# Kernel optimization log

Measured on AMD Instinct MI355X. Metric: run time of the kernel, lower is better.

## Reference

```python
import jax, jax.numpy as jnp
import numpy as np

B, S, D, F, E, K = 4, 2048, 512, 2048, 8, 2


def setup_inputs() -> dict:
    key = jax.random.key(0)
    kx, kg, kw, kv, k2 = jax.random.split(key, 5)
    scale = 0.02
    return {
        "x": jax.random.normal(kx, (B, S, D), dtype=jnp.float32),
        "Wg": jax.random.normal(kg, (D, E), dtype=jnp.float32) * scale,
        "W": jax.random.normal(kw, (E, D, F), dtype=jnp.float32) * scale,
        "V": jax.random.normal(kv, (E, D, F), dtype=jnp.float32) * scale,
        "W2": jax.random.normal(k2, (E, F, D), dtype=jnp.float32) * scale,
    }


def reference(x, Wg, W, V, W2):
    # Gating: top-k over expert logits, softmax over the selected k logits.
    gate_logits = jnp.einsum("bsd,de->bse", x, Wg)                 # [B,S,E]
    topv, topi = jax.lax.top_k(gate_logits, K)                      # [B,S,K]
    w = jax.nn.softmax(topv, axis=-1)                               # [B,S,K]
    # Dense per-token combine weights: gw[b,s,e] = sum_k w[b,s,k]*[topi[b,s,k]==e]
    gw = jnp.sum(w[..., None] * jax.nn.one_hot(topi, E, dtype=x.dtype), axis=-2)  # [B,S,E]

    y = jnp.zeros_like(x)
    n_experts = W.shape[0]
    for e in range(n_experts):  # fixed small loop over experts
        h = jax.nn.silu(jnp.einsum("bsd,df->bsf", x, W[e])) * jnp.einsum("bsd,df->bsf", x, V[e])
        y = y + gw[..., e:e + 1] * jnp.einsum("bsf,fd->bsd", h, W2[e])
    return y
```

## Files before the change

kernel.cpp:

```cpp
#include <hip/hip_runtime.h>
#include <hip/hip_bf16.h>
#include <stdint.h>

#define TT 8192
#define DD 512
#define FF 2048
#define EE 8
#define MAXT 136

typedef __attribute__((ext_vector_type(8))) short bf16x8;
typedef __attribute__((ext_vector_type(4))) float f32x4;

static __device__ __forceinline__ unsigned short f2b(float f) {
  union { __hip_bfloat16 b; unsigned short u; } cv;
  cv.b = __float2bfloat16(f);
  return cv.u;
}

static __device__ __forceinline__ void gload16(const void* g, void* l) {
  __builtin_amdgcn_global_load_lds(
      (const __attribute__((address_space(1))) unsigned int*)g,
      (__attribute__((address_space(3))) unsigned int*)l, 16, 0, 0);
}

__launch_bounds__(256)
__global__ void k_prep(const float* __restrict__ x, const float* __restrict__ Wg,
                       unsigned short* __restrict__ xb,
                       int* __restrict__ te, float* __restrict__ tw) {
  int wid = threadIdx.x >> 6, lane = threadIdx.x & 63;
  int t = blockIdx.x * 4 + wid;
  const float* xr = x + (size_t)t * DD;
  unsigned short* xbr = xb + (size_t)t * DD;
  int d0 = lane * 8;

  float4 v0 = *(const float4*)(xr + d0);
  float4 v1 = *(const float4*)(xr + d0 + 4);
  ushort4 o0, o1;
  o0.x = f2b(v0.x); o0.y = f2b(v0.y); o0.z = f2b(v0.z); o0.w = f2b(v0.w);
  o1.x = f2b(v1.x); o1.y = f2b(v1.y); o1.z = f2b(v1.z); o1.w = f2b(v1.w);
  *(ushort4*)(xbr + d0) = o0;
  *(ushort4*)(xbr + d0 + 4) = o1;

  float xv[8] = {v0.x, v0.y, v0.z, v0.w, v1.x, v1.y, v1.z, v1.w};
  float acc[EE];
#pragma unroll
  for (int e = 0; e < EE; e++) acc[e] = 0.f;
#pragma unroll
  for (int j = 0; j < 8; j++) {
    const float* wg = Wg + (size_t)(d0 + j) * EE;
    float4 a = *(const float4*)wg;
    float4 b = *(const float4*)(wg + 4);
    acc[0] += xv[j] * a.x; acc[1] += xv[j] * a.y; acc[2] += xv[j] * a.z; acc[3] += xv[j] * a.w;
    acc[4] += xv[j] * b.x; acc[5] += xv[j] * b.y; acc[6] += xv[j] * b.z; acc[7] += xv[j] * b.w;
  }
#pragma unroll
  for (int e = 0; e < EE; e++)
    for (int o = 32; o; o >>= 1) acc[e] += __shfl_xor(acc[e], o);
  if (lane == 0) {
    int e1 = 0; float v1m = acc[0];
#pragma unroll
    for (int e = 1; e < EE; e++) if (acc[e] > v1m) { v1m = acc[e]; e1 = e; }
    int e2 = -1; float v2m = -INFINITY;
#pragma unroll
    for (int e = 0; e < EE; e++) if (e != e1 && acc[e] > v2m) { v2m = acc[e]; e2 = e; }
    float ex = __expf(v2m - v1m);
    float w1 = 1.f / (1.f + ex);
    float w2 = ex / (1.f + ex);
    te[t * 2] = e1; te[t * 2 + 1] = e2;
    tw[t * 2] = w1; tw[t * 2 + 1] = w2;
  }
}

__global__ void k_tcvt_all(const float* __restrict__ W, const float* __restrict__ V,
                           const float* __restrict__ W2, unsigned short* __restrict__ Wt,
                           unsigned short* __restrict__ Vt, unsigned short* __restrict__ W2t) {
  __shared__ float tile[32][33];
  int z = blockIdx.y;
  const float* src; unsigned short* dst; int N, nbx;
  if (z < 16) {
    int e = z & 7;
    size_t base = (size_t)e * DD * FF;
    src = (z < 8 ? W : V) + base;
    dst = (z < 8 ? Wt : Vt) + base;
    N = FF; nbx = FF / 32;
  } else {
    int e = z - 16;
    size_t base = (size_t)e * DD * FF;
    src = W2 + base; dst = W2t + base;
    N = DD; nbx = DD / 32;
  }
  int M = (z < 16) ? DD : FF;
  int bx = blockIdx.x;
  int cb = (bx % nbx) * 32, rb = (bx / nbx) * 32;
  int tx = threadIdx.x, ty = threadIdx.y;
#pragma unroll
  for (int i = 0; i < 4; i++)
    tile[ty + i * 8][tx] = src[(size_t)(rb + ty + i * 8) * N + cb + tx];
  __syncthreads();
#pragma unroll
  for (int i = 0; i < 4; i++)
    dst[(size_t)(cb + ty + i * 8) * M + rb + tx] = f2b(tile[tx][ty + i * 8]);
}

__launch_bounds__(1024)
__global__ void k_route(const int* __restrict__ te, const float* __restrict__ tw,
                        int* __restrict__ ctrl, int* __restrict__ perm,
                        float* __restrict__ pw, int* __restrict__ tileE,
                        int* __restrict__ tileRow, int* __restrict__ inv) {
  __shared__ int wsum[17][EE];
  __shared__ int ebase[EE];
  int tid = threadIdx.x;
  int lane = tid & 63, wid = tid >> 6;
  int myte[16]; float mytw[16];
  int c[EE];
#pragma unroll
  for (int e = 0; e < EE; e++) c[e] = 0;
  int s0 = tid * 16;
#pragma unroll
  for (int j = 0; j < 16; j++) {
    myte[j] = te[s0 + j];
    mytw[j] = tw[s0 + j];
#pragma unroll
    for (int e = 0; e < EE; e++) if (myte[j] == e) c[e]++;
  }
  int incl[EE];
#pragma unroll
  for (int e = 0; e < EE; e++) incl[e] = c[e];
  for (int off = 1; off < 64; off <<= 1) {
#pragma unroll
    for (int e = 0; e < EE; e++) {
      int v = __shfl_up(incl[e], off);
      if (lane >= off) incl[e] += v;
    }
  }
  if (lane == 63)
#pragma unroll
    for (int e = 0; e < EE; e++) wsum[wid][e] = incl[e];
  __syncthreads();
  if (tid < EE) {
    int s = 0;
    for (int w = 0; w < 16; w++) { int v = wsum[w][tid]; wsum[w][tid] = s; s += v; }
    wsum[16][tid] = s;
  }
  __syncthreads();
  if (tid == 0) {
    int s = 0, nt = 0;
    for (int e = 0; e < EE; e++) {
      int cnt = wsum[16][e];
      ebase[e] = s; ctrl[8 + e] = s; ctrl[e] = cnt;
      for (int i = 0; i < cnt; i += 128) { tileE[nt] = e; tileRow[nt] = s + i; nt++; }
      s += cnt;
    }
    ctrl[16] = s; ctrl[17] = nt;
  }
  __syncthreads();
#pragma unroll
  for (int e = 0; e < EE; e++) {
    int p = ebase[e] + wsum[wid][e] + incl[e] - c[e];
#pragma unroll
    for (int j = 0; j < 16; j++) {
      if (myte[j] == e) {
        perm[p] = (s0 + j) >> 1;
        pw[p] = mytw[j];
        inv[s0 + j] = p;
        p++;
      }
    }
  }
}

__launch_bounds__(256, 2)
__global__ void k_ffn1(const unsigned short* __restrict__ xb,
                       const unsigned short* __restrict__ Wt,
                       const unsigned short* __restrict__ Vt,
                       const int* __restrict__ perm, const float* __restrict__ pw,
                       const int* __restrict__ ctrl, const int* __restrict__ tileE,
                       const int* __restrict__ tileRow,
                       unsigned short* __restrict__ h) {
  int ti = blockIdx.y;
  if (ti >= ctrl[17]) return;
  int e = tileE[ti];
  int row0 = tileRow[ti];
  int last = ctrl[8 + e] + ctrl[e] - 1;
  int f0 = blockIdx.x * 128;

  __shared__ __align__(16) short As[2][128 * 32];
  __shared__ __align__(16) short Bs[2][256 * 32];

  int tid = threadIdx.x;
  int lane = tid & 63, wid = tid >> 6;
  int wr = wid >> 1, wc = wid & 1;

  int sl = (((tid & 3) ^ ((tid >> 3) & 3))) * 8;

  int ar1 = row0 + (tid >> 2); if (ar1 > last) ar1 = last;
  int ar2 = row0 + (tid >> 2) + 64; if (ar2 > last) ar2 = last;
  const unsigned short* agp1 = xb + (size_t)perm[ar1] * DD + sl;
  const unsigned short* agp2 = xb + (size_t)perm[ar2] * DD + sl;
  const unsigned short* wgp1 = Wt + ((size_t)e * FF + f0 + (tid >> 2)) * DD + sl;
  const unsigned short* wgp2 = wgp1 + (size_t)64 * DD;
  const unsigned short* vgp1 = Vt + ((size_t)e * FF + f0 + (tid >> 2)) * DD + sl;
  const unsigned short* vgp2 = vgp1 + (size_t)64 * DD;

#define STAGE1(buf, k0) do { \
    gload16(agp1 + (k0), &As[buf][tid * 8]); \
    gload16(agp2 + (k0), &As[buf][(tid + 256) * 8]); \
    gload16(wgp1 + (k0), &Bs[buf][tid * 8]); \
    gload16(wgp2 + (k0), &Bs[buf][(tid + 256) * 8]); \
    gload16(vgp1 + (k0), &Bs[buf][(tid + 512) * 8]); \
    gload16(vgp2 + (k0), &Bs[buf][(tid + 768) * 8]); \
  } while (0)

  f32x4 zz = {0.f, 0.f, 0.f, 0.f};
  f32x4 accw[4][4], accv[4][4];
#pragma unroll
  for (int m = 0; m < 4; m++)
#pragma unroll
    for (int n = 0; n < 4; n++) { accw[m][n] = zz; accv[m][n] = zz; }

  int lrow = lane & 15;
  int jx = (((lane >> 4) ^ ((lane >> 1) & 3))) * 8;

#define COMP1(buf) do { \
    bf16x8 a[4], bw[4], bv[4]; \
    _Pragma("unroll") \
    for (int m = 0; m < 4; m++) a[m] = *(bf16x8*)&As[buf][(wr * 64 + m * 16 + lrow) * 32 + jx]; \
    _Pragma("unroll") \
    for (int n = 0; n < 4; n++) { \
      bw[n] = *(bf16x8*)&Bs[buf][(wc * 64 + n * 16 + lrow) * 32 + jx]; \
      bv[n] = *(bf16x8*)&Bs[buf][(128 + wc * 64 + n * 16 + lrow) * 32 + jx]; \
    } \
    _Pragma("unroll") \
    for (int m = 0; m < 4; m++) \
      _Pragma("unroll") \
      for (int n = 0; n < 4; n++) { \
        accw[m][n] = __builtin_amdgcn_mfma_f32_16x16x32_bf16(a[m], bw[n], accw[m][n], 0, 0, 0); \
        accv[m][n] = __builtin_amdgcn_mfma_f32_16x16x32_bf16(a[m], bv[n], accv[m][n], 0, 0, 0); \
      } \
  } while (0)

  STAGE1(0, 0);
  __syncthreads();
#pragma unroll 1
  for (int ks = 0; ks < 16; ks += 2) {
    if (ks + 1 < 16) STAGE1(1, (ks + 1) * 32);
    COMP1(0);
    __syncthreads();
    if (ks + 2 < 16) STAGE1(0, (ks + 2) * 32);
    COMP1(1);
    __syncthreads();
  }
#undef STAGE1
#undef COMP1

#pragma unroll
  for (int m = 0; m < 4; m++) {
    int rbase = row0 + wr * 64 + m * 16 + (lane >> 4) * 4;
#pragma unroll
    for (int reg = 0; reg < 4; reg++) {
      int r = rbase + reg;
      if (r > last) continue;
      float pwv = pw[r];
      size_t hrow = (size_t)r * FF;
#pragma unroll
      for (int n = 0; n < 4; n++) {
        float a = accw[m][n][reg];
        float b = accv[m][n][reg];
        float hv = a / (1.f + __expf(-a)) * b * pwv;
        h[hrow + f0 + wc * 64 + n * 16 + lrow] = f2b(hv);
      }
    }
  }
}

__launch_bounds__(256)
__global__ void k_ffn2(const unsigned short* __restrict__ h,
                       const unsigned short* __restrict__ W2t,
                       const int* __restrict__ ctrl,
                       const int* __restrict__ tileE, const int* __restrict__ tileRow,
                       float* __restrict__ yp) {
  int ti = blockIdx.y;
  if (ti >= ctrl[17]) return;
  int e = tileE[ti];
  int row0 = tileRow[ti];
  int last = ctrl[8 + e] + ctrl[e] - 1;
  int d0 = blockIdx.x * 128;

  __shared__ __align__(16) short As[2][128 * 32];
  __shared__ __align__(16) short Bs[2][128 * 32];

  int tid = threadIdx.x;
  int lane = tid & 63, wid = tid >> 6;
  int wm = (wid >> 1) * 64, wn = (wid & 1) * 64;

  int sl = (((tid & 3) ^ ((tid >> 3) & 3))) * 8;

  int ar1 = row0 + (tid >> 2); if (ar1 > last) ar1 = last;
  int ar2 = row0 + (tid >> 2) + 64; if (ar2 > last) ar2 = last;
  const unsigned short* agp1 = h + (size_t)ar1 * FF + sl;
  const unsigned short* agp2 = h + (size_t)ar2 * FF + sl;
  const unsigned short* bgp1 = W2t + ((size_t)e * DD + d0 + (tid >> 2)) * FF + sl;
  const unsigned short* bgp2 = bgp1 + (size_t)64 * FF;

#define STAGE2(buf, k0) do { \
    gload16(agp1 + (k0), &As[buf][tid * 8]); \
    gload16(agp2 + (k0), &As[buf][(tid + 256) * 8]); \
    gload16(bgp1 + (k0), &Bs[buf][tid * 8]); \
    gload16(bgp2 + (k0), &Bs[buf][(tid + 256) * 8]); \
  } while (0)

  f32x4 zz = {0.f, 0.f, 0.f, 0.f};
  f32x4 acc[4][4];
#pragma unroll
  for (int m = 0; m < 4; m++)
#pragma unroll
    for (int n = 0; n < 4; n++) acc[m][n] = zz;

  int lrow = lane & 15;
  int jx = (((lane >> 4) ^ ((lane >> 1) & 3))) * 8;

#define COMP2(buf) do { \
    bf16x8 a[4], b[4]; \
    _Pragma("unroll") \
    for (int m = 0; m < 4; m++) a[m] = *(bf16x8*)&As[buf][(wm + m * 16 + lrow) * 32 + jx]; \
    _Pragma("unroll") \
    for (int n = 0; n < 4; n++) b[n] = *(bf16x8*)&Bs[buf][(wn + n * 16 + lrow) * 32 + jx]; \
    _Pragma("unroll") \
    for (int m = 0; m < 4; m++) \
      _Pragma("unroll") \
      for (int n = 0; n < 4; n++) \
        acc[m][n] = __builtin_amdgcn_mfma_f32_16x16x32_bf16(a[m], b[n], acc[m][n], 0, 0, 0); \
  } while (0)

  STAGE2(0, 0);
  __syncthreads();
#pragma unroll 1
  for (int ks = 0; ks < 64; ks += 2) {
    if (ks + 1 < 64) STAGE2(1, (ks + 1) * 32);
    COMP2(0);
    __syncthreads();
    if (ks + 2 < 64) STAGE2(0, (ks + 2) * 32);
    COMP2(1);
    __syncthreads();
  }
#undef STAGE2
#undef COMP2

#pragma unroll
  for (int m = 0; m < 4; m++) {
    int rbase = row0 + wm + m * 16 + (lane >> 4) * 4;
#pragma unroll
    for (int reg = 0; reg < 4; reg++) {
      int r = rbase + reg;
      if (r > last) continue;
      float* ypr = yp + (size_t)r * DD + d0;
#pragma unroll
      for (int n = 0; n < 4; n++)
        ypr[wn + n * 16 + lrow] = acc[m][n][reg];
    }
  }
}

__launch_bounds__(256)
__global__ void k_gather(const float4* __restrict__ yp4, const int* __restrict__ inv,
                         float4* __restrict__ y4) {
  int i = blockIdx.x * 256 + threadIdx.x;
  int t = i >> 7, c = i & 127;
  int pa = inv[2 * t], pb = inv[2 * t + 1];
  float4 a = yp4[(size_t)pa * 128 + c];
  float4 b = yp4[(size_t)pb * 128 + c];
  float4 o;
  o.x = a.x + b.x; o.y = a.y + b.y; o.z = a.z + b.z; o.w = a.w + b.w;
  y4[i] = o;
}

extern "C" void kernel_launch(void* const* d_in, const int* in_sizes, int n_in,
                              void* d_out, int out_size, void* d_ws, size_t ws_size,
                              hipStream_t stream) {
  const float* x  = (const float*)d_in[0];
  const float* Wg = (const float*)d_in[1];
  const float* W  = (const float*)d_in[2];
  const float* V  = (const float*)d_in[3];
  const float* W2 = (const float*)d_in[4];
  float* y = (float*)d_out;

  char* ws = (char*)d_ws;
  size_t off = 0;
  auto alloc = [&](size_t n) -> char* {
    char* p = ws + off;
    off += (n + 255) & ~(size_t)255;
    return p;
  };
  unsigned short* xb  = (unsigned short*)alloc((size_t)TT * DD * 2);
  unsigned short* Wt  = (unsigned short*)alloc((size_t)EE * DD * FF * 2);
  unsigned short* Vt  = (unsigned short*)alloc((size_t)EE * DD * FF * 2);
  unsigned short* W2t = (unsigned short*)alloc((size_t)EE * DD * FF * 2);
  unsigned short* h   = (unsigned short*)alloc((size_t)TT * 2 * FF * 2);
  int*   perm = (int*)alloc(TT * 2 * 4);
  float* pw   = (float*)alloc(TT * 2 * 4);
  int*   te   = (int*)alloc(TT * 2 * 4);
  float* tw   = (float*)alloc(TT * 2 * 4);
  int*   inv  = (int*)alloc(TT * 2 * 4);
  int*   ctrl = (int*)alloc(256);
  int*   tileE   = (int*)alloc(MAXT * 4);
  int*   tileRow = (int*)alloc(MAXT * 4);
  if (off > ws_size) return;

  float* yp = (float*)Wt;

  k_prep<<<TT / 4, 256, 0, stream>>>(x, Wg, xb, te, tw);
  k_tcvt_all<<<dim3(1024, 24), dim3(32, 8), 0, stream>>>(W, V, W2, Wt, Vt, W2t);
  k_route<<<1, 1024, 0, stream>>>(te, tw, ctrl, perm, pw, tileE, tileRow, inv);
  k_ffn1<<<dim3(FF / 128, MAXT), 256, 0, stream>>>(xb, Wt, Vt, perm, pw, ctrl, tileE, tileRow, h);
  k_ffn2<<<dim3(DD / 128, MAXT), 256, 0, stream>>>(h, W2t, ctrl, tileE, tileRow, yp);
  k_gather<<<TT * 128 / 256, 256, 0, stream>>>((const float4*)yp, inv, (float4*)y);
}
```

Measured before the change: 253.0 us.

## Use explicit vmcnt waits and raw barriers in GEMM loops; widen transpose tiles

Both grouped GEMM main loops now issue the next stage's global-to-LDS loads first, then wait with a partial s_waitcnt vmcnt so only the current buffer's loads must land before the barrier. This replaces __syncthreads, which drains all outstanding loads, and is meant to overlap memory traffic with MFMA work. s_setprio is raised around the MFMA block. The weight transpose/convert kernel moves to 64x64 tiles with float4 loads and 16-byte bf16 stores. The hand-set vmcnt counts must match the exact number of loads issued per stage, or the loop reads stale LDS data.

```diff
diff --git a/kernel.cpp b/kernel.cpp
--- a/kernel.cpp
+++ b/kernel.cpp
@@ -22,6 +22,11 @@
       (const __attribute__((address_space(1))) unsigned int*)g,
       (__attribute__((address_space(3))) unsigned int*)l, 16, 0, 0);
 }
+
+#define VMCNT6 asm volatile("s_waitcnt vmcnt(6)" ::: "memory")
+#define VMCNT4 asm volatile("s_waitcnt vmcnt(4)" ::: "memory")
+#define VMCNT0 asm volatile("s_waitcnt vmcnt(0)" ::: "memory")
+#define BARX   asm volatile("s_barrier" ::: "memory")
 
 __launch_bounds__(256)
 __global__ void k_prep(const float* __restrict__ x, const float* __restrict__ Wg,
@@ -71,35 +76,47 @@
   }
 }
 
+__launch_bounds__(256)
 __global__ void k_tcvt_all(const float* __restrict__ W, const float* __restrict__ V,
                            const float* __restrict__ W2, unsigned short* __restrict__ Wt,
                            unsigned short* __restrict__ Vt, unsigned short* __restrict__ W2t) {
-  __shared__ float tile[32][33];
+  __shared__ float tile[64][65];
   int z = blockIdx.y;
-  const float* src; unsigned short* dst; int N, nbx;
+  const float* src; unsigned short* dst; int M, N;
   if (z < 16) {
     int e = z & 7;
     size_t base = (size_t)e * DD * FF;
     src = (z < 8 ? W : V) + base;
     dst = (z < 8 ? Wt : Vt) + base;
-    N = FF; nbx = FF / 32;
+    M = DD; N = FF;
   } else {
     int e = z - 16;
     size_t base = (size_t)e * DD * FF;
     src = W2 + base; dst = W2t + base;
-    N = DD; nbx = DD / 32;
-  }
-  int M = (z < 16) ? DD : FF;
+    M = FF; N = DD;
+  }
+  int nbx = N >> 6;
   int bx = blockIdx.x;
-  int cb = (bx % nbx) * 32, rb = (bx / nbx) * 32;
-  int tx = threadIdx.x, ty = threadIdx.y;
-#pragma unroll
-  for (int i = 0; i < 4; i++)
-    tile[ty + i * 8][tx] = src[(size_t)(rb + ty + i * 8) * N + cb + tx];
+  int cb = (bx % nbx) * 64, rb = (bx / nbx) * 64;
+  int t = threadIdx.x;
+#pragma unroll
+  for (int i = 0; i < 4; i++) {
+    int idx = i * 256 + t;
+    int r = idx >> 4, cblk = (idx & 15) * 4;
+    float4 v = *(const float4*)(src + (size_t)(rb + r) * N + cb + cblk);
+    tile[r][cblk] = v.x; tile[r][cblk + 1] = v.y;
+    tile[r][cblk + 2] = v.z; tile[r][cblk + 3] = v.w;
+  }
   __syncthreads();
 #pragma unroll
-  for (int i = 0; i < 4; i++)
-    dst[(size_t)(cb + ty + i * 8) * M + rb + tx] = f2b(tile[tx][ty + i * 8]);
+  for (int j = 0; j < 2; j++) {
+    int idx = j * 256 + t;
+    int c = idx >> 3, seg = (idx & 7) * 8;
+    bf16x8 o;
+#pragma unroll
+    for (int k = 0; k < 8; k++) o[k] = (short)f2b(tile[seg + k][c]);
+    *(bf16x8*)(dst + (size_t)(cb + c) * M + rb + seg) = o;
+  }
 }
 
 __launch_bounds__(1024)
@@ -230,6 +247,7 @@
       bw[n] = *(bf16x8*)&Bs[buf][(wc * 64 + n * 16 + lrow) * 32 + jx]; \
       bv[n] = *(bf16x8*)&Bs[buf][(128 + wc * 64 + n * 16 + lrow) * 32 + jx]; \
     } \
+    __builtin_amdgcn_s_setprio(1); \
     _Pragma("unroll") \
     for (int m = 0; m < 4; m++) \
       _Pragma("unroll") \
@@ -237,18 +255,20 @@
         accw[m][n] = __builtin_amdgcn_mfma_f32_16x16x32_bf16(a[m], bw[n], accw[m][n], 0, 0, 0); \
         accv[m][n] = __builtin_amdgcn_mfma_f32_16x16x32_bf16(a[m], bv[n], accv[m][n], 0, 0, 0); \
       } \
+    __builtin_amdgcn_s_setprio(0); \
   } while (0)
 
   STAGE1(0, 0);
-  __syncthreads();
 #pragma unroll 1
   for (int ks = 0; ks < 16; ks += 2) {
-    if (ks + 1 < 16) STAGE1(1, (ks + 1) * 32);
+    STAGE1(1, (ks + 1) * 32);
+    VMCNT6; BARX;
     COMP1(0);
-    __syncthreads();
-    if (ks + 2 < 16) STAGE1(0, (ks + 2) * 32);
+    BARX;
+    if (ks + 2 < 16) { STAGE1(0, (ks + 2) * 32); VMCNT6; } else { VMCNT0; }
+    BARX;
     COMP1(1);
-    __syncthreads();
+    BARX;
   }
 #undef STAGE1
 #undef COMP1
@@ -325,23 +345,26 @@
     for (int m = 0; m < 4; m++) a[m] = *(bf16x8*)&As[buf][(wm + m * 16 + lrow) * 32 + jx]; \
     _Pragma("unroll") \
     for (int n = 0; n < 4; n++) b[n] = *(bf16x8*)&Bs[buf][(wn + n * 16 + lrow) * 32 + jx]; \
+    __builtin_amdgcn_s_setprio(1); \
     _Pragma("unroll") \
     for (int m = 0; m < 4; m++) \
       _Pragma("unroll") \
       for (int n = 0; n < 4; n++) \
         acc[m][n] = __builtin_amdgcn_mfma_f32_16x16x32_bf16(a[m], b[n], acc[m][n], 0, 0, 0); \
+    __builtin_amdgcn_s_setprio(0); \
   } while (0)
 
   STAGE2(0, 0);
-  __syncthreads();
 #pragma unroll 1
   for (int ks = 0; ks < 64; ks += 2) {
-    if (ks + 1 < 64) STAGE2(1, (ks + 1) * 32);
+    STAGE2(1, (ks + 1) * 32);
+    VMCNT4; BARX;
     COMP2(0);
-    __syncthreads();
-    if (ks + 2 < 64) STAGE2(0, (ks + 2) * 32);
+    BARX;
+    if (ks + 2 < 64) { STAGE2(0, (ks + 2) * 32); VMCNT4; } else { VMCNT0; }
+    BARX;
     COMP2(1);
-    __syncthreads();
+    BARX;
   }
 #undef STAGE2
 #undef COMP2
@@ -409,7 +432,7 @@
   float* yp = (float*)Wt;
 
   k_prep<<<TT / 4, 256, 0, stream>>>(x, Wg, xb, te, tw);
-  k_tcvt_all<<<dim3(1024, 24), dim3(32, 8), 0, stream>>>(W, V, W2, Wt, Vt, W2t);
+  k_tcvt_all<<<dim3(256, 24), 256, 0, stream>>>(W, V, W2, Wt, Vt, W2t);
   k_route<<<1, 1024, 0, stream>>>(te, tw, ctrl, perm, pw, tileE, tileRow, inv);
   k_ffn1<<<dim3(FF / 128, MAXT), 256, 0, stream>>>(xb, Wt, Vt, perm, pw, ctrl, tileE, tileRow, h);
   k_ffn2<<<dim3(DD / 128, MAXT), 256, 0, stream>>>(h, W2t, ctrl, tileE, tileRow, yp);
```

Result: slower. 270.6 us (+7.0%).
